# Optimization experiments

Measured on AMD Instinct MI355X. Metric: run time of the kernel, lower is better.

The kernel has to match this reference:

```python
import jax, jax.numpy as jnp
import numpy as np

N_LAT, N_LON = 121, 240
N = N_LAT * N_LON          # 29040 nodes (fixed by module's reshape)
DEG = 16
E = N * DEG                # 464640 edges
H = 128                    # input_nf = output_nf = hidden_nf
LV = 11                    # pressure levels (coord_mlp outputs 11*2)
EDGE_IN = 2 * H + 34       # source + target + w_diff(33) + edge_attr(1)


def setup_inputs() -> dict:
    key = jax.random.key(0)
    ks = jax.random.split(key, 18)
    def w(k, shape, s=0.05):
        return jax.random.normal(k, shape, dtype=jnp.float32) * s
    return {
        'h': w(ks[0], (N, H), 1.0),
        'u': w(ks[1], (N, LV), 1.0),
        'v': w(ks[2], (N, LV), 1.0),
        'edge_attr': w(ks[3], (E, 1), 1.0),
        # edge MLP: Linear(EDGE_IN,H) ReLU Linear(H,H) ReLU
        'W_e1': w(ks[4], (EDGE_IN, H)), 'b_e1': jnp.zeros((H,), jnp.float32),
        'W_e2': w(ks[5], (H, H)),       'b_e2': jnp.zeros((H,), jnp.float32),
        # node MLP: Linear(2H+H,H) ReLU Linear(H,H)
        'W_n1': w(ks[6], (3 * H, H)),   'b_n1': jnp.zeros((H,), jnp.float32),
        'W_n2': w(ks[7], (H, H)),       'b_n2': jnp.zeros((H,), jnp.float32),
        # coord MLP: Linear(H,H) ReLU Linear(H,22,bias=False) with tiny xavier gain
        'W_c1': w(ks[8], (H, H)),       'b_c1': jnp.zeros((H,), jnp.float32),
        'W_cl': w(ks[9], (H, 2 * LV), 0.001),
        'edge_index': jax.random.randint(ks[10], (2, E), 0, N, dtype=jnp.int32),
    }


def reference(h, u, v, edge_attr,
              W_e1, b_e1, W_e2, b_e2,
              W_n1, b_n1, W_n2, b_n2,
              W_c1, b_c1, W_cl,
              edge_index):
    row, col = edge_index[0], edge_index[1]

    # ---- coord2radial ----
    uc, vc = u[col], v[col]          # [E, LV]
    ur, vr = u[row], v[row]
    col_speed = jnp.sqrt(uc * uc + vc * vc)
    row_speed = jnp.sqrt(ur * ur + vr * vr)
    rel_dirt = (uc * ur + vc * vr) / (col_speed * row_speed)
    w_diff = jnp.concatenate([rel_dirt, col_speed, row_speed], axis=1)  # [E, 33]

    # ---- edge model ----
    edge_in = jnp.concatenate([h[row], h[col], w_diff, edge_attr], axis=1)  # [E, EDGE_IN]
    edge_feat = jax.nn.relu(jax.nn.relu(edge_in @ W_e1 + b_e1) @ W_e2 + b_e2)  # [E, H]

    # ---- node model (scatter-sum + lat-band mean pooling) ----
    agg = jax.ops.segment_sum(edge_feat, row, num_segments=N)  # [N, H]
    lat = agg.reshape(N_LAT, N_LON, H).mean(axis=1, keepdims=True)  # [121,1,H]
    lat_agg = jnp.broadcast_to(lat, (N_LAT, N_LON, H)).reshape(N, H)
    node_in = jnp.concatenate([h, agg, lat_agg], axis=1)  # [N, 3H]
    h_out = jax.nn.relu(node_in @ W_n1 + b_n1) @ W_n2 + b_n2 + h  # residual

    # ---- coord model (scatter-mean with clamp) ----
    ef = (jax.nn.relu(edge_feat @ W_c1 + b_c1) @ W_cl).reshape(E, 2, LV)
    radial = jnp.stack([uc, vc], axis=1)                 # [E, 2, LV]
    rad2 = jnp.sqrt(jnp.sum(radial * radial, axis=-1))   # [E, 2] (per-component magnitude)
    wind = ef * rad2[:, :, None]                         # [E, 2, LV]
    cnt = jnp.maximum(
        jax.ops.segment_sum(jnp.ones((E,), jnp.float32), row, num_segments=N), 1.0)[:, None]
    agg_u = jnp.clip(jax.ops.segment_sum(wind[:, 0, :], row, num_segments=N) / cnt, -100.0, 100.0)
    agg_v = jnp.clip(jax.ops.segment_sum(wind[:, 1, :], row, num_segments=N) / cnt, -100.0, 100.0)

    return h_out, agg_u, agg_v
```

## Files before the change

kernel.cpp:

```cpp
#include <hip/hip_runtime.h>
#include <hip/hip_bf16.h>
#include <math.h>

#define NN   29040
#define NLAT 121
#define NLON 240
#define HD   128
#define LVN  11
#define EE   464640

typedef __attribute__((ext_vector_type(8))) short short8;
typedef __attribute__((ext_vector_type(16))) float f16v;

#define OFF_WE1 0
#define OFF_WE2 40960
#define OFF_WC1 57344
#define OFF_WCL 73728
#define OFF_WN1 77824
#define OFF_WN2 126976
#define WP_SHORTS 143360

__device__ inline short f2b(float x) {
    union { __hip_bfloat16 b; short s; } v;
    v.b = __float2bfloat16(x);
    return v.s;
}
__device__ inline float b2f(unsigned short b) {
    union { unsigned u; float f; } v; v.u = ((unsigned)b) << 16;
    return v.f;
}
__device__ inline unsigned pk2(float lo, float hi) {
    return ((unsigned)(unsigned short)f2b(hi) << 16) | (unsigned short)f2b(lo);
}
__device__ inline float asf(unsigned u) {
    union { unsigned u; float f; } v; v.u = u;
    return v.f;
}

__global__ __launch_bounds__(256)
void hist_kernel(const int* __restrict__ eidx, int* __restrict__ cnt)
{
    int e = blockIdx.x * 256 + threadIdx.x;
    atomicAdd(&cnt[eidx[e]], 1);
}

__global__ __launch_bounds__(1024)
void scan_kernel(const int* __restrict__ cnt, int* __restrict__ off)
{
    __shared__ int part[1024];
    const int tid = threadIdx.x;
    const int CH = 29;
    int lo = tid * CH, hi = min(lo + CH, NN);
    int s = 0;
    for (int i = lo; i < hi; ++i) s += cnt[i];
    part[tid] = s;
    __syncthreads();
    for (int d = 1; d < 1024; d <<= 1) {
        int vv = (tid >= d) ? part[tid - d] : 0;
        __syncthreads();
        part[tid] += vv;
        __syncthreads();
    }
    int run = (tid == 0) ? 0 : part[tid - 1];
    for (int i = lo; i < hi; ++i) { off[i] = run; run += cnt[i]; }
    if (tid == 1023) off[NN] = run;
}

#define SS_SCAT  1815
#define SS_HCAST 1815
#define SS_UV    114
#define SS_WP    70

__global__ __launch_bounds__(256)
void scatter_setup(const int* __restrict__ eidx, const float* __restrict__ ea,
                   const int* __restrict__ off, int* __restrict__ cur,
                   int* __restrict__ rows_r, int* __restrict__ cols_r,
                   float* __restrict__ ear,
                   const float* __restrict__ h, short* __restrict__ hb,
                   const float* __restrict__ u, const float* __restrict__ v,
                   short* __restrict__ uvb,
                   const float* __restrict__ We1, const float* __restrict__ We2,
                   const float* __restrict__ Wc1, const float* __restrict__ Wcl,
                   const float* __restrict__ Wn1, const float* __restrict__ Wn2,
                   short* __restrict__ wp)
{
    const int b = blockIdx.x, tid = threadIdx.x;
    if (b < SS_SCAT) {
        int e = b * 256 + tid;
        int row = eidx[e];
        int col = eidx[EE + e];
        float a = ea[e];
        int p = atomicAdd(&cur[row], 1);
        int idx = off[row] + p;
        rows_r[idx] = row;
        cols_r[idx] = col;
        ear[idx] = a;
        return;
    }
    if (b < SS_SCAT + SS_HCAST) {
        int idx = (b - SS_SCAT) * 256 + tid;
        const float4* hf = (const float4*)h;
        float4 a = hf[idx * 2], c = hf[idx * 2 + 1];
        short8 o;
        o[0] = f2b(a.x); o[1] = f2b(a.y); o[2] = f2b(a.z); o[3] = f2b(a.w);
        o[4] = f2b(c.x); o[5] = f2b(c.y); o[6] = f2b(c.z); o[7] = f2b(c.w);
        ((short8*)hb)[idx] = o;
        return;
    }
    if (b < SS_SCAT + SS_HCAST + SS_UV) {
        int n = (b - SS_SCAT - SS_HCAST) * 256 + tid;
        if (n >= NN) return;
        short* r = uvb + (size_t)n * 40;
        float un = 0.f, vn = 0.f;
#pragma unroll
        for (int l = 0; l < LVN; ++l) {
            float uu = u[n * LVN + l], vv = v[n * LVN + l];
            float s = sqrtf(uu * uu + vv * vv);
            r[l]      = f2b(uu / s);
            r[11 + l] = f2b(vv / s);
            r[22 + l] = f2b(s);
            un += uu * uu; vn += vv * vv;
        }
        r[33] = f2b(sqrtf(un));
        r[34] = f2b(sqrtf(vn));
        r[35] = 0; r[36] = 0; r[37] = 0; r[38] = 0; r[39] = 0;
        return;
    }
    {
        int fg = (b - SS_SCAT - SS_HCAST - SS_UV) * 4 + (tid >> 6);
        const int l = tid & 63;
        int kind, f, base;
        if (fg < 80)       { kind = 0; f = fg;       base = OFF_WE1; }
        else if (fg < 112) { kind = 1; f = fg - 80;  base = OFF_WE2; }
        else if (fg < 144) { kind = 2; f = fg - 112; base = OFF_WC1; }
        else if (fg < 152) { kind = 3; f = fg - 144; base = OFF_WCL; }
        else if (fg < 248) { kind = 4; f = fg - 152; base = OFF_WN1; }
        else               { kind = 5; f = fg - 248; base = OFF_WN2; }
        const int nfw = (kind == 3) ? 1 : 4;
        const int kf = f / nfw, nf = f % nfw;
        const bool perm = (kind == 1) || (kind == 2) || (kind == 3) || (kind == 5);
        short* dst = wp + base + (size_t)f * 512 + l * 8;
        for (int i = 0; i < 8; ++i) {
            int kp = kf * 16 + ((l >> 5) << 3) + i;
            int k;
            if (perm) { int s6 = kp & 63; k = (kp & 64) + (s6 >> 1) + ((s6 & 1) << 5); }
            else k = kp;
            int n = nf * 32 + (l & 31);
            float val = 0.f;
            if (kind == 0) {
                int r = (k < 33) ? (256 + k) : (k == 33 ? 289 : (k < 64 ? -1 : k - 64));
                if (r >= 0) val = We1[r * HD + n];
            } else if (kind == 1) val = We2[k * HD + n];
            else if (kind == 2)  val = Wc1[k * HD + n];
            else if (kind == 3)  { if (n < 22) val = Wcl[k * 22 + n]; }
            else if (kind == 4)  val = Wn1[k * HD + n];
            else                 val = Wn2[k * HD + n];
            dst[i] = f2b(val);
        }
    }
}

template<int KF, int NFL, int NJ>
__device__ inline void gemm32_lds(const short* At, const short* Wp, int nf0,
                                  const float* bias, f16v* acc,
                                  int mrow, int colbase, int r31, int kh, int lane)
{
    const char* arow = (const char*)At + mrow * 256;
    const int sw = (mrow & 7) << 4;
#pragma unroll
    for (int j = 0; j < NJ; ++j) {
        float bv = bias ? bias[colbase + j * 32 + r31] : 0.f;
#pragma unroll
        for (int q = 0; q < 16; ++q) acc[j][q] = bv;
    }
#pragma unroll
    for (int kf = 0; kf < KF; ++kf) {
        short8 a = *(const short8*)(arow + ((kf * 32 + 16 * kh) ^ sw));
#pragma unroll
        for (int j = 0; j < NJ; ++j) {
            short8 bfr = *(const short8*)(Wp + (size_t)(kf * NFL + nf0 + j) * 512 + lane * 8);
            acc[j] = __builtin_amdgcn_mfma_f32_32x32x16_bf16(a, bfr, acc[j], 0, 0, 0);
        }
    }
}

__device__ inline void store_pk32(short* tile, const f16v* acc, int rg, int cg,
                                  int r31, int kh, bool relu)
{
    const int boff = cg * 128 + r31 * 4;
#pragma unroll
    for (int reg = 0; reg < 16; ++reg) {
        int row = rg * 32 + (reg & 3) + 8 * (reg >> 2) + 4 * kh;
        float lo = acc[0][reg], hi = acc[1][reg];
        if (relu) { lo = fmaxf(lo, 0.f); hi = fmaxf(hi, 0.f); }
        *(unsigned*)((char*)tile + row * 256 + (boff ^ ((row & 7) << 4))) = pk2(lo, hi);
    }
}

__global__ __launch_bounds__(256, 4)
void edge_mfma(const short* __restrict__ hb, const short* __restrict__ uvb,
               const int* __restrict__ rows_r, const int* __restrict__ cols_r,
               const float* __restrict__ ear,
               const float* __restrict__ be1, const float* __restrict__ be2,
               const float* __restrict__ bc1,
               const short* __restrict__ wp,
               float* __restrict__ agg, float* __restrict__ aggu,
               float* __restrict__ aggv)
{
    __shared__ short Twd[64 * 64];
    __shared__ short T1[64 * 128];
    __shared__ int   rows_s[64];
    __shared__ float radu_s[64], radv_s[64];

    const int tid = threadIdx.x, lane = tid & 63, w = tid >> 6;
    const int rg = w >> 1, cg = w & 1;
    const int bid = blockIdx.x;
    const int xcd = bid & 7, o = bid >> 3;
    const int tbase = (xcd < 4) ? xcd * 908 : 4 * 908 + (xcd - 4) * 907;
    const int e0 = (tbase + o) * 64;
    const int r31 = lane & 31, kh = lane >> 5;
    const int mrow = rg * 32 + r31;
    const int sw = (mrow & 7) << 4;
    const int colbase = cg * 64;

    int rowm = rows_r[e0 + mrow], colm = cols_r[e0 + mrow];
    const short* hr = hb + (size_t)rowm * HD + 8 * kh;
    const short* hc = hb + (size_t)colm * HD + 8 * kh;

    {
        const int m2 = tid >> 2, q = tid & 3;
        const int sw2 = (m2 & 7) << 4;
        int row2 = rows_r[e0 + m2], col2 = cols_r[e0 + m2];
        const short* rc = uvb + (size_t)col2 * 40;
        const short* rr = uvb + (size_t)row2 * 40;
        char* arow = (char*)(Twd + m2 * 64);
        short8 z = {0, 0, 0, 0, 0, 0, 0, 0};
        *(short8*)(arow + q * 32) = z;
        *(short8*)(arow + q * 32 + 16) = z;
        for (int l = q; l < LVN; l += 4) {
            float rel = b2f((unsigned short)rc[l]) * b2f((unsigned short)rr[l])
                      + b2f((unsigned short)rc[11 + l]) * b2f((unsigned short)rr[11 + l]);
            *(short*)(arow + ((2 * l) ^ sw2))        = f2b(rel);
            *(short*)(arow + ((2 * (11 + l)) ^ sw2)) = rc[22 + l];
            *(short*)(arow + ((2 * (22 + l)) ^ sw2)) = rr[22 + l];
        }
        if (q == 0) {
            rows_s[m2] = row2;
            radu_s[m2] = b2f((unsigned short)rc[33]);
            radv_s[m2] = b2f((unsigned short)rc[34]);
        }
        if (q == 3) *(short*)(arow + ((2 * 33) ^ sw2)) = f2b(ear[e0 + m2]);
    }
    __syncthreads();

    f16v acc[2];
#pragma unroll
    for (int j = 0; j < 2; ++j) {
        float bv = be1[colbase + j * 32 + r31];
#pragma unroll
        for (int q = 0; q < 16; ++q) acc[j][q] = bv;
    }
    {
        const char* awd = (const char*)(Twd + mrow * 64);
#pragma unroll
        for (int kf = 0; kf < 4; ++kf) {
            short8 a = *(const short8*)(awd + ((kf * 32 + 16 * kh) ^ sw));
#pragma unroll
            for (int j = 0; j < 2; ++j) {
                short8 bfr = *(const short8*)(wp + OFF_WE1 + (size_t)(kf * 4 + cg * 2 + j) * 512 + lane * 8);
                acc[j] = __builtin_amdgcn_mfma_f32_32x32x16_bf16(a, bfr, acc[j], 0, 0, 0);
            }
        }
#pragma unroll
        for (int s = 0; s < 8; ++s) {
            short8 a = *(const short8*)(hr + s * 16);
#pragma unroll
            for (int j = 0; j < 2; ++j) {
                short8 bfr = *(const short8*)(wp + OFF_WE1 + (size_t)((s + 4) * 4 + cg * 2 + j) * 512 + lane * 8);
                acc[j] = __builtin_amdgcn_mfma_f32_32x32x16_bf16(a, bfr, acc[j], 0, 0, 0);
            }
        }
#pragma unroll
        for (int s = 0; s < 8; ++s) {
            short8 a = *(const short8*)(hc + s * 16);
#pragma unroll
            for (int j = 0; j < 2; ++j) {
                short8 bfr = *(const short8*)(wp + OFF_WE1 + (size_t)((s + 12) * 4 + cg * 2 + j) * 512 + lane * 8);
                acc[j] = __builtin_amdgcn_mfma_f32_32x32x16_bf16(a, bfr, acc[j], 0, 0, 0);
            }
        }
    }
    store_pk32(T1, acc, rg, cg, r31, kh, true);
    __syncthreads();

    gemm32_lds<8, 4, 2>(T1, wp + OFF_WE2, cg * 2, be2, acc, mrow, colbase, r31, kh, lane);
    __syncthreads();
    store_pk32(T1, acc, rg, cg, r31, kh, true);
    __syncthreads();

    gemm32_lds<8, 4, 2>(T1, wp + OFF_WC1, cg * 2, bc1, acc, mrow, colbase, r31, kh, lane);

    {
        const int p = cg * 32 + (lane & 31);
        const int rh = lane >> 5;
        const int n0 = (p >> 5) * 64 + (p & 31), n1 = n0 + 32;
        const int m0 = rg * 32 + rh * 16;
        int curr = rows_s[m0];
        float s0 = 0.f, s1 = 0.f;
        for (int m = m0; m < m0 + 16; ++m) {
            int r = rows_s[m];
            unsigned vv = *(const unsigned*)((const char*)T1 + m * 256 + ((4 * p) ^ ((m & 7) << 4)));
            if (r != curr) {
                atomicAdd(&agg[(size_t)curr * HD + n0], s0);
                atomicAdd(&agg[(size_t)curr * HD + n1], s1);
                s0 = 0.f; s1 = 0.f; curr = r;
            }
            s0 += asf(vv << 16);
            s1 += asf(vv & 0xFFFF0000u);
        }
        atomicAdd(&agg[(size_t)curr * HD + n0], s0);
        atomicAdd(&agg[(size_t)curr * HD + n1], s1);
    }
    __syncthreads();
    store_pk32(T1, acc, rg, cg, r31, kh, true);
    __syncthreads();

    if (cg == 0) {
        gemm32_lds<8, 1, 1>(T1, wp + OFF_WCL, 0, (const float*)nullptr, acc, mrow, 0, r31, kh, lane);
        float* O22 = (float*)Twd;
#pragma unroll
        for (int reg = 0; reg < 16; ++reg) {
            int row = rg * 32 + (reg & 3) + 8 * (reg >> 2) + 4 * kh;
            O22[row * 32 + r31] = acc[0][reg];
        }
        const int c = r31;
        if (c < 22) {
            const bool isU = c < LVN;
            const int lvl = isU ? c : c - LVN;
            float* dst = isU ? aggu : aggv;
            const float* radp = isU ? radu_s : radv_s;
            const int m0 = rg * 32 + kh * 16;
            int curr = rows_s[m0]; float s = 0.f;
            for (int m = m0; m < m0 + 16; ++m) {
                int r = rows_s[m];
                float vv = O22[m * 32 + c] * radp[m];
                if (r != curr) { atomicAdd(&dst[(size_t)curr * LVN + lvl], s); s = 0.f; curr = r; }
                s += vv;
            }
            atomicAdd(&dst[(size_t)curr * LVN + lvl], s);
        }
    }
}

__global__ __launch_bounds__(256)
void post_kernel(const float* __restrict__ agg, short* __restrict__ latb)
{
    const int b = blockIdx.x, tid = threadIdx.x;
    __shared__ float part[256];
    const int j = tid & 127, half = tid >> 7;
    float s = 0.f;
    for (int lon = half * 120; lon < (half + 1) * 120; ++lon)
        s += agg[((size_t)b * NLON + lon) * HD + j];
    part[tid] = s;
    __syncthreads();
    if (tid < 128)
        latb[(size_t)b * HD + tid] = f2b((part[tid] + part[128 + tid]) * (1.0f / NLON));
}

__global__ __launch_bounds__(512, 4)
void node_mfma(const short* __restrict__ hb, const float* __restrict__ h,
               const short* __restrict__ latb,
               const float* __restrict__ bn1, const float* __restrict__ bn2,
               const short* __restrict__ wp, float* __restrict__ out,
               float* __restrict__ aggu, float* __restrict__ aggv,
               const int* __restrict__ cnt)
{
    __shared__ short T1[128 * 128];
    const int tid = threadIdx.x, lane = tid & 63, w = tid >> 6;
    const int rg = w >> 1, cg = w & 1;
    const int r31 = lane & 31, kh = lane >> 5;
    const int mrow = rg * 32 + r31;
    const int colbase = cg * 64;
    const int n0 = blockIdx.x * 128;
    const int n = n0 + mrow;
    const int nc = (n < NN) ? n : (NN - 1);
    const short* hp = hb + (size_t)nc * HD + 8 * kh;
    const float* ap = out + (size_t)nc * HD + 8 * kh;
    const short* lp = latb + (size_t)(nc / NLON) * HD + 8 * kh;

    f16v acc[2];
#pragma unroll
    for (int j = 0; j < 2; ++j) {
        float bv = bn1[colbase + j * 32 + r31];
#pragma unroll
        for (int q = 0; q < 16; ++q) acc[j][q] = bv;
    }
#pragma unroll
    for (int s = 0; s < 8; ++s) {
        short8 a = *(const short8*)(hp + s * 16);
#pragma unroll
        for (int j = 0; j < 2; ++j) {
            short8 bfr = *(const short8*)(wp + OFF_WN1 + (size_t)(s * 4 + cg * 2 + j) * 512 + lane * 8);
            acc[j] = __builtin_amdgcn_mfma_f32_32x32x16_bf16(a, bfr, acc[j], 0, 0, 0);
        }
    }
#pragma unroll
    for (int s = 0; s < 8; ++s) {
        short8 a;
#pragma unroll
        for (int q = 0; q < 8; ++q) a[q] = f2b(ap[s * 16 + q]);
#pragma unroll
        for (int j = 0; j < 2; ++j) {
            short8 bfr = *(const short8*)(wp + OFF_WN1 + (size_t)((s + 8) * 4 + cg * 2 + j) * 512 + lane * 8);
            acc[j] = __builtin_amdgcn_mfma_f32_32x32x16_bf16(a, bfr, acc[j], 0, 0, 0);
        }
    }
#pragma unroll
    for (int s = 0; s < 8; ++s) {
        short8 a = *(const short8*)(lp + s * 16);
#pragma unroll
        for (int j = 0; j < 2; ++j) {
            short8 bfr = *(const short8*)(wp + OFF_WN1 + (size_t)((s + 16) * 4 + cg * 2 + j) * 512 + lane * 8);
            acc[j] = __builtin_amdgcn_mfma_f32_32x32x16_bf16(a, bfr, acc[j], 0, 0, 0);
        }
    }
    store_pk32(T1, acc, rg, cg, r31, kh, true);
    __syncthreads();
    gemm32_lds<8, 4, 2>(T1, wp + OFF_WN2, cg * 2, bn2, acc, mrow, colbase, r31, kh, lane);

#pragma unroll
    for (int j = 0; j < 2; ++j)
#pragma unroll
        for (int reg = 0; reg < 16; ++reg) {
            int row = rg * 32 + (reg & 3) + 8 * (reg >> 2) + 4 * kh;
            int gn = n0 + row;
            if (gn < NN) {
                int col = colbase + j * 32 + r31;
                out[(size_t)gn * HD + col] = acc[j][reg] + h[(size_t)gn * HD + col];
            }
        }

    for (int tt = blockIdx.x * 512 + tid; tt < NN * LVN; tt += gridDim.x * 512) {
        int nn2 = tt / LVN;
        float c = fmaxf((float)cnt[nn2], 1.f);
        float xu = aggu[tt] / c, xv = aggv[tt] / c;
        aggu[tt] = fminf(fmaxf(xu, -100.f), 100.f);
        aggv[tt] = fminf(fmaxf(xv, -100.f), 100.f);
    }
}

extern "C" void kernel_launch(void* const* d_in, const int* in_sizes, int n_in,
                              void* d_out, int out_size, void* d_ws, size_t ws_size,
                              hipStream_t stream)
{
    const float* h   = (const float*)d_in[0];
    const float* u   = (const float*)d_in[1];
    const float* v   = (const float*)d_in[2];
    const float* ea  = (const float*)d_in[3];
    const float* We1 = (const float*)d_in[4];
    const float* be1 = (const float*)d_in[5];
    const float* We2 = (const float*)d_in[6];
    const float* be2 = (const float*)d_in[7];
    const float* Wn1 = (const float*)d_in[8];
    const float* bn1 = (const float*)d_in[9];
    const float* Wn2 = (const float*)d_in[10];
    const float* bn2 = (const float*)d_in[11];
    const float* Wc1 = (const float*)d_in[12];
    const float* bc1 = (const float*)d_in[13];
    const float* Wcl = (const float*)d_in[14];
    const int*   eidx = (const int*)d_in[15];

    float* out  = (float*)d_out;
    float* agg  = out;
    float* aggu = out + (size_t)NN * HD;
    float* aggv = aggu + (size_t)NN * LVN;

    char* p = (char*)d_ws;
    short* wp  = (short*)p;                  p += (size_t)WP_SHORTS * 2;
    int*   off = (int*)p;                    p += (size_t)(NN + 1) * 4;
    p = (char*)(((size_t)p + 15) & ~(size_t)15);
    short* hb  = (short*)p;                  p += (size_t)NN * HD * 2;
    short* uvb = (short*)p;                  p += (size_t)NN * 40 * 2;
    short* latb = (short*)p;                 p += (size_t)NLAT * HD * 2;
    p = (char*)(((size_t)p + 15) & ~(size_t)15);
    int*   rows_r = (int*)p;                 p += (size_t)EE * 4;
    int*   cols_r = (int*)p;                 p += (size_t)EE * 4;
    float* ear    = (float*)p;               p += (size_t)EE * 4;
    p = (char*)(((size_t)p + 15) & ~(size_t)15);
    int*   cnt = (int*)p;                    p += (size_t)NN * 4;
    int*   cur = (int*)p;

    hipMemsetAsync(d_out, 0, (size_t)out_size * sizeof(float), stream);
    hipMemsetAsync(cnt, 0, (size_t)2 * NN * sizeof(int), stream);

    hist_kernel<<<EE / 256, 256, 0, stream>>>(eidx, cnt);
    scan_kernel<<<1, 1024, 0, stream>>>(cnt, off);
    scatter_setup<<<SS_SCAT + SS_HCAST + SS_UV + SS_WP, 256, 0, stream>>>(
        eidx, ea, off, cur, rows_r, cols_r, ear,
        h, hb, u, v, uvb, We1, We2, Wc1, Wcl, Wn1, Wn2, wp);

    edge_mfma<<<EE / 64, 256, 0, stream>>>(hb, uvb, rows_r, cols_r, ear,
                                           be1, be2, bc1, wp, agg, aggu, aggv);

    post_kernel<<<NLAT, 256, 0, stream>>>(agg, latb);

    node_mfma<<<(NN + 127) / 128, 512, 0, stream>>>(hb, h, latb, bn1, bn2, wp,
                                                    agg, aggu, aggv, cnt);
}
```

Baseline: 284.6 us.

## Fuse lat-band mean into node kernel and zero aggregation buffer in hist kernel

Removes the separate lat-band pooling kernel: each node block now reduces the one or two latitude bands it covers directly from a workspace aggregation buffer into shared memory. The edge kernel accumulates into this workspace buffer, which hist_kernel zeroes, so the large output memset shrinks to only the coordinate outputs. This trades a kernel launch and a large memset for redundant per-block band reductions that serialize before the node MFMA work.

```diff
diff --git a/kernel.cpp b/kernel.cpp
--- a/kernel.cpp
+++ b/kernel.cpp
@@ -38,9 +38,13 @@
 }
 
 __global__ __launch_bounds__(256)
-void hist_kernel(const int* __restrict__ eidx, int* __restrict__ cnt)
+void hist_kernel(const int* __restrict__ eidx, int* __restrict__ cnt,
+                 float* __restrict__ aggw)
 {
     int e = blockIdx.x * 256 + threadIdx.x;
+    float4 z = {0.f, 0.f, 0.f, 0.f};
+    ((float4*)aggw)[e * 2]     = z;
+    ((float4*)aggw)[e * 2 + 1] = z;
     atomicAdd(&cnt[eidx[e]], 1);
 }
 
@@ -352,30 +356,17 @@
     }
 }
 
-__global__ __launch_bounds__(256)
-void post_kernel(const float* __restrict__ agg, short* __restrict__ latb)
-{
-    const int b = blockIdx.x, tid = threadIdx.x;
-    __shared__ float part[256];
-    const int j = tid & 127, half = tid >> 7;
-    float s = 0.f;
-    for (int lon = half * 120; lon < (half + 1) * 120; ++lon)
-        s += agg[((size_t)b * NLON + lon) * HD + j];
-    part[tid] = s;
-    __syncthreads();
-    if (tid < 128)
-        latb[(size_t)b * HD + tid] = f2b((part[tid] + part[128 + tid]) * (1.0f / NLON));
-}
-
 __global__ __launch_bounds__(512, 4)
 void node_mfma(const short* __restrict__ hb, const float* __restrict__ h,
-               const short* __restrict__ latb,
+               const float* __restrict__ aggw,
                const float* __restrict__ bn1, const float* __restrict__ bn2,
                const short* __restrict__ wp, float* __restrict__ out,
                float* __restrict__ aggu, float* __restrict__ aggv,
                const int* __restrict__ cnt)
 {
     __shared__ short T1[128 * 128];
+    __shared__ float latS[2 * 128];
+    __shared__ short latB[2 * 128];
     const int tid = threadIdx.x, lane = tid & 63, w = tid >> 6;
     const int rg = w >> 1, cg = w & 1;
     const int r31 = lane & 31, kh = lane >> 5;
@@ -384,9 +375,27 @@
     const int n0 = blockIdx.x * 128;
     const int n = n0 + mrow;
     const int nc = (n < NN) ? n : (NN - 1);
+
+    const int b0 = n0 / NLON;
+    const int b1 = min((n0 + 127) / NLON, NLAT - 1);
+    for (int i = tid; i < 256; i += 512) latS[i] = 0.f;
+    __syncthreads();
+    {
+        const int col = tid & 127, part = (tid >> 7) & 3;
+        for (int band = b0; band <= b1; ++band) {
+            const float* ap2 = aggw + ((size_t)band * NLON + part * 60) * HD + col;
+            float s = 0.f;
+            for (int lon = 0; lon < 60; ++lon) s += ap2[(size_t)lon * HD];
+            atomicAdd(&latS[(band - b0) * 128 + col], s);
+        }
+    }
+    __syncthreads();
+    for (int i = tid; i < 256; i += 512) latB[i] = f2b(latS[i] * (1.0f / NLON));
+    __syncthreads();
+
     const short* hp = hb + (size_t)nc * HD + 8 * kh;
-    const float* ap = out + (size_t)nc * HD + 8 * kh;
-    const short* lp = latb + (size_t)(nc / NLON) * HD + 8 * kh;
+    const float* ap = aggw + (size_t)nc * HD + 8 * kh;
+    const short* lp = latB + (nc / NLON - b0) * 128 + 8 * kh;
 
     f16v acc[2];
 #pragma unroll
@@ -471,7 +480,6 @@
     const int*   eidx = (const int*)d_in[15];
 
     float* out  = (float*)d_out;
-    float* agg  = out;
     float* aggu = out + (size_t)NN * HD;
     float* aggv = aggu + (size_t)NN * LVN;
 
@@ -481,8 +489,8 @@
     p = (char*)(((size_t)p + 15) & ~(size_t)15);
     short* hb  = (short*)p;                  p += (size_t)NN * HD * 2;
     short* uvb = (short*)p;                  p += (size_t)NN * 40 * 2;
-    short* latb = (short*)p;                 p += (size_t)NLAT * HD * 2;
     p = (char*)(((size_t)p + 15) & ~(size_t)15);
+    float* aggw = (float*)p;                 p += (size_t)NN * HD * 4;
     int*   rows_r = (int*)p;                 p += (size_t)EE * 4;
     int*   cols_r = (int*)p;                 p += (size_t)EE * 4;
     float* ear    = (float*)p;               p += (size_t)EE * 4;
@@ -490,20 +498,18 @@
     int*   cnt = (int*)p;                    p += (size_t)NN * 4;
     int*   cur = (int*)p;
 
-    hipMemsetAsync(d_out, 0, (size_t)out_size * sizeof(float), stream);
+    hipMemsetAsync(aggu, 0, (size_t)2 * NN * LVN * sizeof(float), stream);
     hipMemsetAsync(cnt, 0, (size_t)2 * NN * sizeof(int), stream);
 
-    hist_kernel<<<EE / 256, 256, 0, stream>>>(eidx, cnt);
+    hist_kernel<<<EE / 256, 256, 0, stream>>>(eidx, cnt, aggw);
     scan_kernel<<<1, 1024, 0, stream>>>(cnt, off);
     scatter_setup<<<SS_SCAT + SS_HCAST + SS_UV + SS_WP, 256, 0, stream>>>(
         eidx, ea, off, cur, rows_r, cols_r, ear,
         h, hb, u, v, uvb, We1, We2, Wc1, Wcl, Wn1, Wn2, wp);
 
     edge_mfma<<<EE / 64, 256, 0, stream>>>(hb, uvb, rows_r, cols_r, ear,
-                                           be1, be2, bc1, wp, agg, aggu, aggv);
-
-    post_kernel<<<NLAT, 256, 0, stream>>>(agg, latb);
-
-    node_mfma<<<(NN + 127) / 128, 512, 0, stream>>>(hb, h, latb, bn1, bn2, wp,
-                                                    agg, aggu, aggv, cnt);
-}
+                                           be1, be2, bc1, wp, aggw, aggu, aggv);
+
+    node_mfma<<<(NN + 127) / 128, 512, 0, stream>>>(hb, h, aggw, bn1, bn2, wp,
+                                                    out, aggu, aggv, cnt);
+}
```

After: 286.6 us. About the same (+0.7%).
